# Kernel optimization log

Hardware: AMD Instinct MI355X
Metric: run time of the kernel (lower is better)

Reference implementation:

```python
import jax, jax.numpy as jnp
import numpy as np

OBS_DIM = 512
BACKBONE_DIMS = [1024, 1024, 512]
EXPERT_HIDDEN = 256
NUM_EXPERTS = 16
NUM_ACTIONS = 32
BATCH = 65536


def _glorot(key, shape):
    fan_in = shape[-2] if len(shape) >= 2 else shape[-1]
    return jax.random.normal(key, shape, dtype=jnp.float32) * (1.0 / np.sqrt(fan_in))


def setup_inputs() -> dict:
    key = jax.random.key(0)
    ks = jax.random.split(key, 16)
    inp = {}
    inp['obs'] = jax.random.normal(ks[0], (BATCH, OBS_DIM), dtype=jnp.float32)
    # shared backbone: 512->1024->1024->512 (Linear+ReLU+Dropout(eval=identity))
    dims = [OBS_DIM] + BACKBONE_DIMS
    for i in range(3):
        inp[f'Wb{i}'] = _glorot(ks[1 + i], (dims[i], dims[i + 1]))
        inp[f'bb{i}'] = jnp.zeros((dims[i + 1],), dtype=jnp.float32)
    # experts, batched over expert dim: 512->256->ReLU->256->32
    inp['We1'] = _glorot(ks[4], (NUM_EXPERTS, BACKBONE_DIMS[-1], EXPERT_HIDDEN))
    inp['be1'] = jnp.zeros((NUM_EXPERTS, EXPERT_HIDDEN), dtype=jnp.float32)
    inp['We2'] = _glorot(ks[5], (NUM_EXPERTS, EXPERT_HIDDEN, NUM_ACTIONS))
    inp['be2'] = jnp.zeros((NUM_EXPERTS, NUM_ACTIONS), dtype=jnp.float32)
    # motion selector: 512->256->128->16 + softmax
    inp['Ws0'] = _glorot(ks[6], (OBS_DIM, 256))
    inp['bs0'] = jnp.zeros((256,), dtype=jnp.float32)
    inp['Ws1'] = _glorot(ks[7], (256, 128))
    inp['bs1'] = jnp.zeros((128,), dtype=jnp.float32)
    inp['Ws2'] = _glorot(ks[8], (128, NUM_EXPERTS))
    inp['bs2'] = jnp.zeros((NUM_EXPERTS,), dtype=jnp.float32)
    return inp


def reference(obs, Wb0, bb0, Wb1, bb1, Wb2, bb2, We1, be1, We2, be2,
              Ws0, bs0, Ws1, bs1, Ws2, bs2):
    # shared backbone (Dropout is identity in eval/inference)
    h = jax.nn.relu(obs @ Wb0 + bb0)
    h = jax.nn.relu(h @ Wb1 + bb1)
    h = jax.nn.relu(h @ Wb2 + bb2)  # [B, 512]
    # all experts on shared features, as one batched GEMM
    eh = jax.nn.relu(jnp.einsum('bd,edh->beh', h, We1) + be1)       # [B, E, 256]
    expert_actions = jnp.einsum('beh,eha->bea', eh, We2) + be2       # [B, E, A]
    # motion selector (softmax fusion weights)
    s = jax.nn.relu(obs @ Ws0 + bs0)
    s = jax.nn.relu(s @ Ws1 + bs1)
    w = jax.nn.softmax(s @ Ws2 + bs2, axis=-1)                        # [B, E]
    # softmax-weighted fusion over experts
    fused = jnp.einsum('bea,be->ba', expert_actions, w)              # [B, A]
    return fused
```

## Files before the change

### kernel.cpp

```cpp
#include <hip/hip_runtime.h>
#include <hip/hip_bf16.h>
#include <stdint.h>

typedef __attribute__((ext_vector_type(8))) short short8;
typedef __attribute__((ext_vector_type(4))) float f32x4;

__device__ __forceinline__ float b2f(short s) {
    union { unsigned u; float f; } v; v.u = ((unsigned)(unsigned short)s) << 16; return v.f;
}
__device__ __forceinline__ short f2b(float f) {
    union { float f; unsigned u; } v; v.f = f;
    unsigned r = (v.u + 0x7FFF + ((v.u >> 16) & 1)) >> 16;
    return (short)r;
}

__device__ __forceinline__ void gload16(const void* g, void* l) {
    __builtin_amdgcn_global_load_lds(
        (const __attribute__((address_space(1))) void*)(uintptr_t)g,
        (__attribute__((address_space(3))) void*)(uintptr_t)l,
        16, 0, 0);
}

#define BAR()    asm volatile("s_barrier" ::: "memory")
#define WAITV2() asm volatile("s_waitcnt vmcnt(2)" ::: "memory")
#define WAITV0() asm volatile("s_waitcnt vmcnt(0)" ::: "memory")
#define WAITL0() asm volatile("s_waitcnt lgkmcnt(0)" ::: "memory")

__global__ __launch_bounds__(256) void cast_bf16_kernel(
    const float* __restrict__ src, short* __restrict__ dst, int n8) {
    int i = blockIdx.x * 256 + threadIdx.x;
    if (i >= n8) return;
    const float4* s = (const float4*)src + (size_t)i * 2;
    float4 x0 = s[0], x1 = s[1];
    short8 o;
    o[0] = f2b(x0.x); o[1] = f2b(x0.y); o[2] = f2b(x0.z); o[3] = f2b(x0.w);
    o[4] = f2b(x1.x); o[5] = f2b(x1.y); o[6] = f2b(x1.z); o[7] = f2b(x1.w);
    *((short8*)dst + i) = o;
}

__global__ __launch_bounds__(256) void transpose_cast_kernel(
    const float* __restrict__ W, short* __restrict__ Wt, int K, int N, int total) {
    int t = blockIdx.x * 256 + threadIdx.x;
    if (t >= total) return;
    const float* src = W + (size_t)blockIdx.y * K * N;
    short* dst = Wt + (size_t)blockIdx.y * K * N;
    int n = t % N;
    int k0 = (t / N) * 8;
    short8 o;
#pragma unroll
    for (int i = 0; i < 8; i++) o[i] = f2b(src[(size_t)(k0 + i) * N + n]);
    *(short8*)(dst + (size_t)n * K + k0) = o;
}

__global__ __launch_bounds__(256) void repack_We2_kernel(
    const float* __restrict__ We2, short* __restrict__ Bt2) {
    int t = blockIdx.x * 256 + threadIdx.x;
    int h0 = (t & 31) * 8;
    int a = (t >> 5) & 31;
    int e = t >> 10;
    short8 o;
#pragma unroll
    for (int j = 0; j < 8; j++) o[j] = f2b(We2[((size_t)e * 256 + h0 + j) * 32 + a]);
    *(short8*)(Bt2 + (size_t)a * 4096 + e * 256 + h0) = o;
}

__global__ __launch_bounds__(256, 3)
void gemm_bt_bias_relu(const short* __restrict__ A, const short* __restrict__ Bt,
                       const float* __restrict__ bias, short* __restrict__ C,
                       int M, int N, int K) {
    __shared__ __align__(16) short As[128 * 32];
    __shared__ __align__(16) short Bs[128 * 32];
    const int tid = threadIdx.x;
    const int w = tid >> 6, lane = tid & 63;
    const int tm = blockIdx.y * 128, tn = blockIdx.x * 128;
    const int wm = (w & 1) * 64, wn = (w >> 1) * 64;
    const int r = lane & 15, q = lane >> 4, qk = q * 8;

    const int c0 = w * 2, c1 = w * 2 + 1;
    const int srow0 = c0 * 16 + (lane >> 2);
    const int srow1 = c1 * 16 + (lane >> 2);
    const int skk = (lane & 3) * 8;
    const short* gA0 = A + (size_t)(tm + srow0) * K + skk;
    const short* gA1 = A + (size_t)(tm + srow1) * K + skk;
    const short* gB0 = Bt + (size_t)(tn + srow0) * K + skk;
    const short* gB1 = Bt + (size_t)(tn + srow1) * K + skk;
    short* lA0 = &As[c0 * 512]; short* lA1 = &As[c1 * 512];
    short* lB0 = &Bs[c0 * 512]; short* lB1 = &Bs[c1 * 512];

    f32x4 acc[4][4] = {};
    for (int k0 = 0; k0 < K; k0 += 32) {
        gload16(gA0 + k0, lA0);
        gload16(gA1 + k0, lA1);
        gload16(gB0 + k0, lB0);
        gload16(gB1 + k0, lB1);
        __syncthreads();
        short8 a[4], b[4];
#pragma unroll
        for (int i = 0; i < 4; i++) a[i] = *(const short8*)&As[(wm + i * 16 + r) * 32 + qk];
#pragma unroll
        for (int j = 0; j < 4; j++) b[j] = *(const short8*)&Bs[(wn + j * 16 + r) * 32 + qk];
#pragma unroll
        for (int i = 0; i < 4; i++)
#pragma unroll
            for (int j = 0; j < 4; j++)
                acc[i][j] = __builtin_amdgcn_mfma_f32_16x16x32_bf16(a[i], b[j], acc[i][j], 0, 0, 0);
        __syncthreads();
    }
#pragma unroll
    for (int j = 0; j < 4; j++) {
        int col = tn + wn + j * 16 + r;
        float bj = bias[col];
#pragma unroll
        for (int i = 0; i < 4; i++)
#pragma unroll
            for (int rr = 0; rr < 4; rr++) {
                int row = tm + wm + i * 16 + q * 4 + rr;
                float v = fmaxf(acc[i][j][rr] + bj, 0.f);
                C[(size_t)row * N + col] = f2b(v);
            }
    }
}

__global__ __launch_bounds__(256)
void selector_softmax(const short* __restrict__ s1, const short* __restrict__ Ws2t,
                      const float* __restrict__ bs2, float* __restrict__ wsel) {
    int tid = threadIdx.x;
    int row = blockIdx.x * 16 + (tid >> 4);
    int e = tid & 15;
    const short8* a = (const short8*)(s1 + (size_t)row * 128);
    const short8* b = (const short8*)(Ws2t + (size_t)e * 128);
    float acc = bs2[e];
#pragma unroll
    for (int kk = 0; kk < 16; ++kk) {
        short8 av = a[kk], bv = b[kk];
#pragma unroll
        for (int i = 0; i < 8; i++) acc = fmaf(b2f(av[i]), b2f(bv[i]), acc);
    }
    float m = acc;
#pragma unroll
    for (int off = 8; off >= 1; off >>= 1) m = fmaxf(m, __shfl_xor(m, off, 16));
    float ex = __expf(acc - m);
    float s = ex;
#pragma unroll
    for (int off = 8; off >= 1; off >>= 1) s += __shfl_xor(s, off, 16);
    wsel[(size_t)row * 16 + e] = ex / s;
}

template<int MODE>
__global__ __launch_bounds__(512, 2)
void gemm256(const short* __restrict__ A, const short* __restrict__ Bt,
             const float* __restrict__ bias, const float* __restrict__ wselp,
             short* __restrict__ C, int M, int N, int K) {
    extern __shared__ __align__(16) short lds[];
    const int tid = threadIdx.x;
    const int w = tid >> 6, lane = tid & 63;
    const int wr = w >> 2, wc = w & 3;

    const int gx = gridDim.x;
    const int b = blockIdx.y * gx + blockIdx.x;
    const int per = (gx * gridDim.y) >> 3;
    const int sb = (b & 7) * per + (b >> 3);
    const int bx = sb % gx, by = sb / gx;
    const int tm = by * 256, tn = bx * 256;

    const int rih = w * 8 + (lane >> 3);
    const int colel = (((lane & 7) ^ (lane >> 3)) << 3);
    const short* pA = A + (size_t)(tm + rih) * K + colel;
    const short* pB = Bt + (size_t)(tn + rih) * K + colel;
    const size_t rK64 = (size_t)64 * K, rK128 = (size_t)128 * K;
    short* const ldsw = lds + w * 512;

#define STG_A(buf, h, t) do { \
        const short* s_ = pA + (size_t)(h) * rK128 + (size_t)(t) * 64; \
        short* d_ = ldsw + (buf) * 32768 + (h) * 8192; \
        gload16(s_, d_); \
        gload16(s_ + rK64, d_ + 4096); } while (0)
#define STG_B(buf, h, t) do { \
        const short* s_ = pB + (size_t)(h) * rK128 + (size_t)(t) * 64; \
        short* d_ = ldsw + (buf) * 32768 + 16384 + (h) * 8192; \
        gload16(s_, d_); \
        gload16(s_ + rK64, d_ + 4096); } while (0)

    const int rA = lane & 15;
    const int csw0 = (((lane >> 4) << 4)) ^ ((lane & 7) << 4);
    const int csw1 = (64 + ((lane >> 4) << 4)) ^ ((lane & 7) << 4);
    const char* const ldsB_ = (const char*)lds;
    const int aBase0 = wr * 16384 + rA * 128;
    const int bBase0 = 32768 + (wc >> 1) * 16384 + ((wc & 1) * 64 + rA) * 128;

    f32x4 acc[8][4] = {};
    short8 a[4][2], b0[2][2], b1[2][2];
    const int nt = K >> 6;

    STG_A(0, 0, 0); STG_A(0, 1, 0); STG_B(0, 0, 0); STG_B(0, 1, 0);
    STG_A(1, 0, 1);
    WAITV2(); BAR();

    for (int t = 0; t < nt; ++t) {
        const int cur = t & 1, nxt = cur ^ 1;
        const char* pa = ldsB_ + cur * 65536 + aBase0;
        const char* pb = ldsB_ + cur * 65536 + bBase0;
#pragma unroll
        for (int m = 0; m < 4; m++) {
            a[m][0] = *(const short8*)(pa + m * 2048 + csw0);
            a[m][1] = *(const short8*)(pa + m * 2048 + csw1);
        }
#pragma unroll
        for (int n = 0; n < 2; n++) {
            b0[n][0] = *(const short8*)(pb + n * 2048 + csw0);
            b0[n][1] = *(const short8*)(pb + n * 2048 + csw1);
        }
        if (t + 1 < nt) STG_A(nxt, 1, t + 1);
        BAR(); WAITL0(); __builtin_amdgcn_sched_barrier(0);
        __builtin_amdgcn_s_setprio(1);
#pragma unroll
        for (int m = 0; m < 4; m++)
#pragma unroll
            for (int n = 0; n < 2; n++) {
                acc[m][n] = __builtin_amdgcn_mfma_f32_16x16x32_bf16(a[m][0], b0[n][0], acc[m][n], 0, 0, 0);
                acc[m][n] = __builtin_amdgcn_mfma_f32_16x16x32_bf16(a[m][1], b0[n][1], acc[m][n], 0, 0, 0);
            }
        __builtin_amdgcn_s_setprio(0);
        BAR();
#pragma unroll
        for (int n = 0; n < 2; n++) {
            b1[n][0] = *(const short8*)(pb + (2 + n) * 2048 + csw0);
            b1[n][1] = *(const short8*)(pb + (2 + n) * 2048 + csw1);
        }
        if (t + 1 < nt) STG_B(nxt, 0, t + 1);
        BAR(); WAITL0(); __builtin_amdgcn_sched_barrier(0);
        __builtin_amdgcn_s_setprio(1);
#pragma unroll
        for (int m = 0; m < 4; m++)
#pragma unroll
            for (int n = 0; n < 2; n++) {
                acc[m][2 + n] = __builtin_amdgcn_mfma_f32_16x16x32_bf16(a[m][0], b1[n][0], acc[m][2 + n], 0, 0, 0);
                acc[m][2 + n] = __builtin_amdgcn_mfma_f32_16x16x32_bf16(a[m][1], b1[n][1], acc[m][2 + n], 0, 0, 0);
            }
        __builtin_amdgcn_s_setprio(0);
        BAR();
#pragma unroll
        for (int m = 0; m < 4; m++) {
            a[m][0] = *(const short8*)(pa + (4 + m) * 2048 + csw0);
            a[m][1] = *(const short8*)(pa + (4 + m) * 2048 + csw1);
        }
        if (t + 1 < nt) STG_B(nxt, 1, t + 1);
        BAR(); WAITL0(); __builtin_amdgcn_sched_barrier(0);
        __builtin_amdgcn_s_setprio(1);
#pragma unroll
        for (int m = 0; m < 4; m++)
#pragma unroll
            for (int n = 0; n < 2; n++) {
                acc[4 + m][2 + n] = __builtin_amdgcn_mfma_f32_16x16x32_bf16(a[m][0], b1[n][0], acc[4 + m][2 + n], 0, 0, 0);
                acc[4 + m][2 + n] = __builtin_amdgcn_mfma_f32_16x16x32_bf16(a[m][1], b1[n][1], acc[4 + m][2 + n], 0, 0, 0);
            }
        __builtin_amdgcn_s_setprio(0);
        BAR();
        if (t + 2 < nt) { STG_A(cur, 0, t + 2); WAITV2(); }
        else { WAITV0(); }
        BAR();
        __builtin_amdgcn_s_setprio(1);
#pragma unroll
        for (int m = 0; m < 4; m++)
#pragma unroll
            for (int n = 0; n < 2; n++) {
                acc[4 + m][n] = __builtin_amdgcn_mfma_f32_16x16x32_bf16(a[m][0], b0[n][0], acc[4 + m][n], 0, 0, 0);
                acc[4 + m][n] = __builtin_amdgcn_mfma_f32_16x16x32_bf16(a[m][1], b0[n][1], acc[4 + m][n], 0, 0, 0);
            }
        __builtin_amdgcn_s_setprio(0);
        BAR();
    }
#undef STG_A
#undef STG_B

    float biasv[4];
#pragma unroll
    for (int n = 0; n < 4; n++) biasv[n] = bias[tn + wc * 64 + n * 16 + rA];
    const int q4 = (lane >> 4) * 4;
#pragma unroll
    for (int m = 0; m < 8; m++)
#pragma unroll
        for (int rr = 0; rr < 4; rr++) {
            const int row = tm + wr * 128 + m * 16 + q4 + rr;
            float ws = 1.f;
            if (MODE == 1) ws = wselp[(size_t)row * 16 + (tn >> 8)];
#pragma unroll
            for (int n = 0; n < 4; n++) {
                const int col = tn + wc * 64 + n * 16 + rA;
                float v = fmaxf(acc[m][n][rr] + biasv[n], 0.f);
                if (MODE == 1) v *= ws;
                C[(size_t)row * N + col] = f2b(v);
            }
        }
}

__global__ __launch_bounds__(256)
void fuse_gemm(const short* __restrict__ Aeh, const short* __restrict__ Bt2,
               const float* __restrict__ wsel, const float* __restrict__ be2,
               float* __restrict__ out, int accflag) {
    __shared__ __align__(16) short sA[2][128 * 64];
    const int tid = threadIdx.x;
    const int w = tid >> 6, lane = tid & 63;
    const int tm = blockIdx.x * 128;
    const int rih = w * 8 + (lane >> 3);
    const int colel = (((lane & 7) ^ (lane >> 3)) << 3);
    const short* pA = Aeh + (size_t)(tm + rih) * 2048 + colel;
    const int rA = lane & 15;
    const int csw0 = (((lane >> 4) << 4)) ^ ((lane & 7) << 4);
    const int csw1 = (64 + ((lane >> 4) << 4)) ^ ((lane & 7) << 4);
    const short* pBg = Bt2 + (size_t)rA * 4096 + ((lane >> 4) << 3);

    f32x4 acc[2][2] = {};
#define STG_E(buf, t) do { \
        const short* s_ = pA + (size_t)(t) * 64; \
        short* d_ = &sA[buf][w * 512]; \
        gload16(s_, d_); \
        gload16(s_ + (size_t)32 * 2048, d_ + 2048); \
        gload16(s_ + (size_t)64 * 2048, d_ + 4096); \
        gload16(s_ + (size_t)96 * 2048, d_ + 6144); } while (0)

    const int NT = 32;
    STG_E(0, 0);
    WAITV0(); BAR();
    for (int t = 0; t < NT; ++t) {
        const int cur = t & 1;
        if (t + 1 < NT) STG_E(cur ^ 1, t + 1);
        const char* pa = (const char*)&sA[cur][0] + (w * 32 + rA) * 128;
        short8 av[2][2], bv[2][2];
#pragma unroll
        for (int m = 0; m < 2; m++) {
            av[m][0] = *(const short8*)(pa + m * 2048 + csw0);
            av[m][1] = *(const short8*)(pa + m * 2048 + csw1);
        }
#pragma unroll
        for (int n = 0; n < 2; n++) {
            bv[n][0] = *(const short8*)(pBg + (size_t)n * 16 * 4096 + t * 64);
            bv[n][1] = *(const short8*)(pBg + (size_t)n * 16 * 4096 + t * 64 + 32);
        }
#pragma unroll
        for (int m = 0; m < 2; m++)
#pragma unroll
            for (int n = 0; n < 2; n++) {
                acc[m][n] = __builtin_amdgcn_mfma_f32_16x16x32_bf16(av[m][0], bv[n][0], acc[m][n], 0, 0, 0);
                acc[m][n] = __builtin_amdgcn_mfma_f32_16x16x32_bf16(av[m][1], bv[n][1], acc[m][n], 0, 0, 0);
            }
        WAITL0(); WAITV0(); BAR();
    }
#undef STG_E

    float be2v0[16], be2v1[16];
    if (!accflag) {
#pragma unroll
        for (int e = 0; e < 16; e++) {
            be2v0[e] = be2[e * 32 + rA];
            be2v1[e] = be2[e * 32 + 16 + rA];
        }
    }
    const int q4 = (lane >> 4) * 4;
#pragma unroll
    for (int m = 0; m < 2; m++)
#pragma unroll
        for (int rr = 0; rr < 4; rr++) {
            const int row = tm + w * 32 + m * 16 + q4 + rr;
            float v0 = acc[m][0][rr], v1 = acc[m][1][rr];
            if (!accflag) {
#pragma unroll
                for (int e = 0; e < 16; e++) {
                    float wv = wsel[(size_t)row * 16 + e];
                    v0 = fmaf(wv, be2v0[e], v0);
                    v1 = fmaf(wv, be2v1[e], v1);
                }
                out[(size_t)row * 32 + rA] = v0;
                out[(size_t)row * 32 + 16 + rA] = v1;
            } else {
                out[(size_t)row * 32 + rA] += v0;
                out[(size_t)row * 32 + 16 + rA] += v1;
            }
        }
}

extern "C" void kernel_launch(void* const* d_in, const int* in_sizes, int n_in,
                              void* d_out, int out_size, void* d_ws, size_t ws_size,
                              hipStream_t stream) {
    const float* obs = (const float*)d_in[0];
    const float* Wb0 = (const float*)d_in[1]; const float* bb0 = (const float*)d_in[2];
    const float* Wb1 = (const float*)d_in[3]; const float* bb1 = (const float*)d_in[4];
    const float* Wb2 = (const float*)d_in[5]; const float* bb2 = (const float*)d_in[6];
    const float* We1 = (const float*)d_in[7]; const float* be1 = (const float*)d_in[8];
    const float* We2 = (const float*)d_in[9]; const float* be2 = (const float*)d_in[10];
    const float* Ws0 = (const float*)d_in[11]; const float* bs0 = (const float*)d_in[12];
    const float* Ws1 = (const float*)d_in[13]; const float* bs1 = (const float*)d_in[14];
    const float* Ws2 = (const float*)d_in[15]; const float* bs2 = (const float*)d_in[16];

    const int B = 65536;
    char* ws = (char*)d_ws;
    size_t off = 0;
    auto alloc = [&](size_t bytes) { void* p = ws + off; off += (bytes + 255) & ~(size_t)255; return p; };
    short* obs_bf = (short*)alloc((size_t)B * 512 * 2);
    short* h1     = (short*)alloc((size_t)B * 1024 * 2);
    short* h2     = (short*)alloc((size_t)B * 1024 * 2);
    short* hbuf   = (short*)alloc((size_t)B * 512 * 2);
    short* s0     = (short*)alloc((size_t)B * 256 * 2);
    short* s1     = (short*)alloc((size_t)B * 128 * 2);
    float* wsel   = (float*)alloc((size_t)B * 16 * 4);
    short* Wb0t   = (short*)alloc((size_t)512 * 1024 * 2);
    short* Wb1t   = (short*)alloc((size_t)1024 * 1024 * 2);
    short* Wb2t   = (short*)alloc((size_t)1024 * 512 * 2);
    short* We1t   = (short*)alloc((size_t)16 * 512 * 256 * 2);
    short* Ws0t   = (short*)alloc((size_t)512 * 256 * 2);
    short* Ws1t   = (short*)alloc((size_t)256 * 128 * 2);
    short* Ws2t   = (short*)alloc((size_t)128 * 16 * 2);
    short* Bt2    = (short*)alloc((size_t)32 * 4096 * 2);
    short* s_eh = h1;

    static int inited = 0;
    if (!inited) {
        hipFuncSetAttribute(reinterpret_cast<const void*>(gemm256<0>),
                            hipFuncAttributeMaxDynamicSharedMemorySize, 131072);
        hipFuncSetAttribute(reinterpret_cast<const void*>(gemm256<1>),
                            hipFuncAttributeMaxDynamicSharedMemorySize, 131072);
        inited = 1;
    }

    cast_bf16_kernel<<<(B * 512 / 8 + 255) / 256, 256, 0, stream>>>(obs, obs_bf, B * 512 / 8);
    transpose_cast_kernel<<<dim3((1024 * 512 / 8 + 255) / 256, 1), 256, 0, stream>>>(Wb0, Wb0t, 512, 1024, 1024 * 512 / 8);
    transpose_cast_kernel<<<dim3((1024 * 1024 / 8 + 255) / 256, 1), 256, 0, stream>>>(Wb1, Wb1t, 1024, 1024, 1024 * 1024 / 8);
    transpose_cast_kernel<<<dim3((512 * 1024 / 8 + 255) / 256, 1), 256, 0, stream>>>(Wb2, Wb2t, 1024, 512, 512 * 1024 / 8);
    transpose_cast_kernel<<<dim3((256 * 512 / 8 + 255) / 256, 16), 256, 0, stream>>>(We1, We1t, 512, 256, 256 * 512 / 8);
    transpose_cast_kernel<<<dim3((256 * 512 / 8 + 255) / 256, 1), 256, 0, stream>>>(Ws0, Ws0t, 512, 256, 256 * 512 / 8);
    transpose_cast_kernel<<<dim3((128 * 256 / 8 + 255) / 256, 1), 256, 0, stream>>>(Ws1, Ws1t, 256, 128, 128 * 256 / 8);
    transpose_cast_kernel<<<dim3((16 * 128 / 8 + 255) / 256, 1), 256, 0, stream>>>(Ws2, Ws2t, 128, 16, 16 * 128 / 8);
    repack_We2_kernel<<<64, 256, 0, stream>>>(We2, Bt2);

    gemm256<0><<<dim3(1, B / 256), 512, 131072, stream>>>(obs_bf, Ws0t, bs0, nullptr, s0, B, 256, 512);
    gemm_bt_bias_relu<<<dim3(1, B / 128), 256, 0, stream>>>(s0, Ws1t, bs1, s1, B, 128, 256);
    selector_softmax<<<B / 16, 256, 0, stream>>>(s1, Ws2t, bs2, wsel);

    gemm256<0><<<dim3(4, B / 256), 512, 131072, stream>>>(obs_bf, Wb0t, bb0, nullptr, h1, B, 1024, 512);
    gemm256<0><<<dim3(4, B / 256), 512, 131072, stream>>>(h1, Wb1t, bb1, nullptr, h2, B, 1024, 1024);
    gemm256<0><<<dim3(2, B / 256), 512, 131072, stream>>>(h2, Wb2t, bb2, nullptr, hbuf, B, 512, 1024);

    for (int g = 0; g < 2; ++g) {
        gemm256<1><<<dim3(8, B / 256), 512, 131072, stream>>>(
            hbuf, We1t + (size_t)g * 8 * 256 * 512, be1 + g * 2048, wsel + g * 8,
            s_eh, B, 2048, 512);
        fuse_gemm<<<B / 128, 256, 0, stream>>>(
            s_eh, Bt2 + g * 2048, wsel, be2, (float*)d_out, g);
    }
}
```

Before: 1.127 ms.

## Fuse expert GEMMs into a persistent MoE kernel and trim barriers in gemm256

Replaces the two-pass expert path with a single kernel. That kernel materialises the eh intermediate (B x 4096) and then runs a separate fuse GEMM. The new kernel loops over all 16 experts for each 256-row tile. It computes the first expert layer, stages the ReLU output in LDS, multiplies it by We2 with MFMA, and accumulates the softmax-weighted result directly into the output. The output is pre-initialised with the weighted be2 bias. This removes the large global write and re-read of expert hidden activations. Separately, several s_barriers are dropped from the gemm256 main loop and the next-tile prefetch is moved after the last MFMA block. Dropping those barriers risks LDS races, and the fused kernel launches only 256 blocks, which can limit occupancy.

```diff
diff --git a/kernel.cpp b/kernel.cpp
--- a/kernel.cpp
+++ b/kernel.cpp
@@ -1,6 +1,7 @@
 #include <hip/hip_runtime.h>
 #include <hip/hip_bf16.h>
 #include <stdint.h>
+
 
 typedef __attribute__((ext_vector_type(8))) short short8;
 typedef __attribute__((ext_vector_type(4))) float f32x4;
@@ -25,6 +26,7 @@
 #define WAITV2() asm volatile("s_waitcnt vmcnt(2)" ::: "memory")
 #define WAITV0() asm volatile("s_waitcnt vmcnt(0)" ::: "memory")
 #define WAITL0() asm volatile("s_waitcnt lgkmcnt(0)" ::: "memory")
+#define SGB()    __builtin_amdgcn_sched_barrier(0)
 
 __global__ __launch_bounds__(256) void cast_bf16_kernel(
     const float* __restrict__ src, short* __restrict__ dst, int n8) {
@@ -50,18 +52,6 @@
 #pragma unroll
     for (int i = 0; i < 8; i++) o[i] = f2b(src[(size_t)(k0 + i) * N + n]);
     *(short8*)(dst + (size_t)n * K + k0) = o;
-}
-
-__global__ __launch_bounds__(256) void repack_We2_kernel(
-    const float* __restrict__ We2, short* __restrict__ Bt2) {
-    int t = blockIdx.x * 256 + threadIdx.x;
-    int h0 = (t & 31) * 8;
-    int a = (t >> 5) & 31;
-    int e = t >> 10;
-    short8 o;
-#pragma unroll
-    for (int j = 0; j < 8; j++) o[j] = f2b(We2[((size_t)e * 256 + h0 + j) * 32 + a]);
-    *(short8*)(Bt2 + (size_t)a * 4096 + e * 256 + h0) = o;
 }
 
 __global__ __launch_bounds__(256, 3)
@@ -146,11 +136,22 @@
     wsel[(size_t)row * 16 + e] = ex / s;
 }
 
-template<int MODE>
+__global__ __launch_bounds__(256)
+void out_init_kernel(const float* __restrict__ wsel, const float* __restrict__ be2,
+                     float* __restrict__ out) {
+    int i = blockIdx.x * 256 + threadIdx.x;
+    int row = i >> 5, a = i & 31;
+    const float* wr = wsel + (size_t)row * 16;
+    float acc = 0.f;
+#pragma unroll
+    for (int e = 0; e < 16; e++) acc = fmaf(wr[e], be2[e * 32 + a], acc);
+    out[i] = acc;
+}
+
 __global__ __launch_bounds__(512, 2)
 void gemm256(const short* __restrict__ A, const short* __restrict__ Bt,
-             const float* __restrict__ bias, const float* __restrict__ wselp,
-             short* __restrict__ C, int M, int N, int K) {
+             const float* __restrict__ bias, short* __restrict__ C,
+             int M, int N, int K) {
     extern __shared__ __align__(16) short lds[];
     const int tid = threadIdx.x;
     const int w = tid >> 6, lane = tid & 63;
@@ -181,9 +182,9 @@
         gload16(s_, d_); \
         gload16(s_ + rK64, d_ + 4096); } while (0)
 
-    const int rA = lane & 15;
-    const int csw0 = (((lane >> 4) << 4)) ^ ((lane & 7) << 4);
-    const int csw1 = (64 + ((lane >> 4) << 4)) ^ ((lane & 7) << 4);
+    const int rA = lane & 15, q = lane >> 4;
+    const int csw0 = ((q << 4)) ^ ((lane & 7) << 4);
+    const int csw1 = (64 + (q << 4)) ^ ((lane & 7) << 4);
     const char* const ldsB_ = (const char*)lds;
     const int aBase0 = wr * 16384 + rA * 128;
     const int bBase0 = 32768 + (wc >> 1) * 16384 + ((wc & 1) * 64 + rA) * 128;
@@ -211,7 +212,7 @@
             b0[n][1] = *(const short8*)(pb + n * 2048 + csw1);
         }
         if (t + 1 < nt) STG_A(nxt, 1, t + 1);
-        BAR(); WAITL0(); __builtin_amdgcn_sched_barrier(0);
+        WAITL0(); SGB();
         __builtin_amdgcn_s_setprio(1);
 #pragma unroll
         for (int m = 0; m < 4; m++)
@@ -221,14 +222,13 @@
                 acc[m][n] = __builtin_amdgcn_mfma_f32_16x16x32_bf16(a[m][1], b0[n][1], acc[m][n], 0, 0, 0);
             }
         __builtin_amdgcn_s_setprio(0);
-        BAR();
 #pragma unroll
         for (int n = 0; n < 2; n++) {
             b1[n][0] = *(const short8*)(pb + (2 + n) * 2048 + csw0);
             b1[n][1] = *(const short8*)(pb + (2 + n) * 2048 + csw1);
         }
         if (t + 1 < nt) STG_B(nxt, 0, t + 1);
-        BAR(); WAITL0(); __builtin_amdgcn_sched_barrier(0);
+        WAITL0(); SGB();
         __builtin_amdgcn_s_setprio(1);
 #pragma unroll
         for (int m = 0; m < 4; m++)
@@ -238,14 +238,13 @@
                 acc[m][2 + n] = __builtin_amdgcn_mfma_f32_16x16x32_bf16(a[m][1], b1[n][1], acc[m][2 + n], 0, 0, 0);
             }
         __builtin_amdgcn_s_setprio(0);
-        BAR();
 #pragma unroll
         for (int m = 0; m < 4; m++) {
             a[m][0] = *(const short8*)(pa + (4 + m) * 2048 + csw0);
             a[m][1] = *(const short8*)(pa + (4 + m) * 2048 + csw1);
         }
         if (t + 1 < nt) STG_B(nxt, 1, t + 1);
-        BAR(); WAITL0(); __builtin_amdgcn_sched_barrier(0);
+        WAITL0(); SGB();
         __builtin_amdgcn_s_setprio(1);
 #pragma unroll
         for (int m = 0; m < 4; m++)
@@ -255,10 +254,6 @@
                 acc[4 + m][2 + n] = __builtin_amdgcn_mfma_f32_16x16x32_bf16(a[m][1], b1[n][1], acc[4 + m][2 + n], 0, 0, 0);
             }
         __builtin_amdgcn_s_setprio(0);
-        BAR();
-        if (t + 2 < nt) { STG_A(cur, 0, t + 2); WAITV2(); }
-        else { WAITV0(); }
-        BAR();
         __builtin_amdgcn_s_setprio(1);
 #pragma unroll
         for (int m = 0; m < 4; m++)
@@ -269,6 +264,9 @@
             }
         __builtin_amdgcn_s_setprio(0);
         BAR();
+        if (t + 2 < nt) { STG_A(cur, 0, t + 2); WAITV2(); }
+        else WAITV0();
+        BAR();
     }
 #undef STG_A
 #undef STG_B
@@ -276,107 +274,206 @@
     float biasv[4];
 #pragma unroll
     for (int n = 0; n < 4; n++) biasv[n] = bias[tn + wc * 64 + n * 16 + rA];
-    const int q4 = (lane >> 4) * 4;
+    const int q4 = q * 4;
 #pragma unroll
     for (int m = 0; m < 8; m++)
 #pragma unroll
         for (int rr = 0; rr < 4; rr++) {
             const int row = tm + wr * 128 + m * 16 + q4 + rr;
-            float ws = 1.f;
-            if (MODE == 1) ws = wselp[(size_t)row * 16 + (tn >> 8)];
 #pragma unroll
             for (int n = 0; n < 4; n++) {
                 const int col = tn + wc * 64 + n * 16 + rA;
                 float v = fmaxf(acc[m][n][rr] + biasv[n], 0.f);
-                if (MODE == 1) v *= ws;
                 C[(size_t)row * N + col] = f2b(v);
             }
         }
 }
 
-__global__ __launch_bounds__(256)
-void fuse_gemm(const short* __restrict__ Aeh, const short* __restrict__ Bt2,
-               const float* __restrict__ wsel, const float* __restrict__ be2,
-               float* __restrict__ out, int accflag) {
-    __shared__ __align__(16) short sA[2][128 * 64];
+__global__ __launch_bounds__(512, 2)
+void moe_kernel(const short* __restrict__ hbuf, const short* __restrict__ We1t,
+                const short* __restrict__ We2t, const float* __restrict__ be1,
+                const float* __restrict__ wsel, float* __restrict__ out) {
+    extern __shared__ __align__(16) short lds[];
     const int tid = threadIdx.x;
     const int w = tid >> 6, lane = tid & 63;
-    const int tm = blockIdx.x * 128;
+    const int wr = w >> 2, wc = w & 3;
+    const int b = blockIdx.x;
+    const int sb = (b & 7) * 32 + (b >> 3);
+    const int tm = sb * 256;
+
     const int rih = w * 8 + (lane >> 3);
     const int colel = (((lane & 7) ^ (lane >> 3)) << 3);
-    const short* pA = Aeh + (size_t)(tm + rih) * 2048 + colel;
-    const int rA = lane & 15;
-    const int csw0 = (((lane >> 4) << 4)) ^ ((lane & 7) << 4);
-    const int csw1 = (64 + ((lane >> 4) << 4)) ^ ((lane & 7) << 4);
-    const short* pBg = Bt2 + (size_t)rA * 4096 + ((lane >> 4) << 3);
-
-    f32x4 acc[2][2] = {};
-#define STG_E(buf, t) do { \
-        const short* s_ = pA + (size_t)(t) * 64; \
-        short* d_ = &sA[buf][w * 512]; \
+    const short* pA = hbuf + (size_t)(tm + rih) * 512 + colel;
+    const short* pB0 = We1t + (size_t)rih * 512 + colel;
+    short* const ldsw = lds + w * 512;
+
+#define MSTG_A(buf, h, t) do { \
+        const short* s_ = pA + (size_t)(h) * 65536 + (size_t)(t) * 64; \
+        short* d_ = ldsw + (buf) * 32768 + (h) * 8192; \
         gload16(s_, d_); \
-        gload16(s_ + (size_t)32 * 2048, d_ + 2048); \
-        gload16(s_ + (size_t)64 * 2048, d_ + 4096); \
-        gload16(s_ + (size_t)96 * 2048, d_ + 6144); } while (0)
-
-    const int NT = 32;
-    STG_E(0, 0);
-    WAITV0(); BAR();
-    for (int t = 0; t < NT; ++t) {
-        const int cur = t & 1;
-        if (t + 1 < NT) STG_E(cur ^ 1, t + 1);
-        const char* pa = (const char*)&sA[cur][0] + (w * 32 + rA) * 128;
-        short8 av[2][2], bv[2][2];
-#pragma unroll
-        for (int m = 0; m < 2; m++) {
-            av[m][0] = *(const short8*)(pa + m * 2048 + csw0);
-            av[m][1] = *(const short8*)(pa + m * 2048 + csw1);
-        }
-#pragma unroll
-        for (int n = 0; n < 2; n++) {
-            bv[n][0] = *(const short8*)(pBg + (size_t)n * 16 * 4096 + t * 64);
-            bv[n][1] = *(const short8*)(pBg + (size_t)n * 16 * 4096 + t * 64 + 32);
-        }
-#pragma unroll
-        for (int m = 0; m < 2; m++)
+        gload16(s_ + 32768, d_ + 4096); } while (0)
+#define MSTG_B(P, buf, h, t) do { \
+        const short* s_ = (P) + (size_t)(h) * 65536 + (size_t)(t) * 64; \
+        short* d_ = ldsw + (buf) * 32768 + 16384 + (h) * 8192; \
+        gload16(s_, d_); \
+        gload16(s_ + 32768, d_ + 4096); } while (0)
+
+    const int rA = lane & 15, q = lane >> 4;
+    const int csw0 = ((q << 4)) ^ ((lane & 7) << 4);
+    const int csw1 = (64 + (q << 4)) ^ ((lane & 7) << 4);
+    const char* const ldsB_ = (const char*)lds;
+    const int aBase0 = wr * 16384 + rA * 128;
+    const int bBase0 = 32768 + (wc >> 1) * 16384 + ((wc & 1) * 64 + rA) * 128;
+    const int q4 = q * 4;
+
+    short8 a[4][2], b0[2][2], b1[2][2];
+
+    {
+        const short* pBe = pB0;
+        MSTG_A(0, 0, 0); MSTG_A(0, 1, 0);
+        MSTG_B(pBe, 0, 0, 0); MSTG_B(pBe, 0, 1, 0);
+    }
+
+#pragma unroll 1
+    for (int e = 0; e < 16; ++e) {
+        const short* pBe = pB0 + (size_t)e * 131072;
+        WAITV0(); BAR();
+        f32x4 acc[8][4] = {};
+#pragma unroll 1
+        for (int t = 0; t < 8; ++t) {
+            const int cur = t & 1, nxt = cur ^ 1;
+            const char* pa = ldsB_ + cur * 65536 + aBase0;
+            const char* pb = ldsB_ + cur * 65536 + bBase0;
+#pragma unroll
+            for (int m = 0; m < 4; m++) {
+                a[m][0] = *(const short8*)(pa + m * 2048 + csw0);
+                a[m][1] = *(const short8*)(pa + m * 2048 + csw1);
+            }
 #pragma unroll
             for (int n = 0; n < 2; n++) {
-                acc[m][n] = __builtin_amdgcn_mfma_f32_16x16x32_bf16(av[m][0], bv[n][0], acc[m][n], 0, 0, 0);
-                acc[m][n] = __builtin_amdgcn_mfma_f32_16x16x32_bf16(av[m][1], bv[n][1], acc[m][n], 0, 0, 0);
-            }
-        WAITL0(); WAITV0(); BAR();
-    }
-#undef STG_E
-
-    float be2v0[16], be2v1[16];
-    if (!accflag) {
-#pragma unroll
-        for (int e = 0; e < 16; e++) {
-            be2v0[e] = be2[e * 32 + rA];
-            be2v1[e] = be2[e * 32 + 16 + rA];
-        }
-    }
-    const int q4 = (lane >> 4) * 4;
-#pragma unroll
-    for (int m = 0; m < 2; m++)
-#pragma unroll
-        for (int rr = 0; rr < 4; rr++) {
-            const int row = tm + w * 32 + m * 16 + q4 + rr;
-            float v0 = acc[m][0][rr], v1 = acc[m][1][rr];
-            if (!accflag) {
-#pragma unroll
-                for (int e = 0; e < 16; e++) {
-                    float wv = wsel[(size_t)row * 16 + e];
-                    v0 = fmaf(wv, be2v0[e], v0);
-                    v1 = fmaf(wv, be2v1[e], v1);
-                }
-                out[(size_t)row * 32 + rA] = v0;
-                out[(size_t)row * 32 + 16 + rA] = v1;
-            } else {
-                out[(size_t)row * 32 + rA] += v0;
-                out[(size_t)row * 32 + 16 + rA] += v1;
-            }
-        }
+                b0[n][0] = *(const short8*)(pb + n * 2048 + csw0);
+                b0[n][1] = *(const short8*)(pb + n * 2048 + csw1);
+            }
+            if (t < 7) MSTG_A(nxt, 1, t + 1);
+            if (t == 0) MSTG_A(nxt, 0, 1);
+            WAITL0(); SGB();
+            __builtin_amdgcn_s_setprio(1);
+#pragma unroll
+            for (int m = 0; m < 4; m++)
+#pragma unroll
+                for (int n = 0; n < 2; n++) {
+                    acc[m][n] = __builtin_amdgcn_mfma_f32_16x16x32_bf16(a[m][0], b0[n][0], acc[m][n], 0, 0, 0);
+                    acc[m][n] = __builtin_amdgcn_mfma_f32_16x16x32_bf16(a[m][1], b0[n][1], acc[m][n], 0, 0, 0);
+                }
+            __builtin_amdgcn_s_setprio(0);
+#pragma unroll
+            for (int n = 0; n < 2; n++) {
+                b1[n][0] = *(const short8*)(pb + (2 + n) * 2048 + csw0);
+                b1[n][1] = *(const short8*)(pb + (2 + n) * 2048 + csw1);
+            }
+            if (t < 7) MSTG_B(pBe, nxt, 0, t + 1);
+            WAITL0(); SGB();
+            __builtin_amdgcn_s_setprio(1);
+#pragma unroll
+            for (int m = 0; m < 4; m++)
+#pragma unroll
+                for (int n = 0; n < 2; n++) {
+                    acc[m][2 + n] = __builtin_amdgcn_mfma_f32_16x16x32_bf16(a[m][0], b1[n][0], acc[m][2 + n], 0, 0, 0);
+                    acc[m][2 + n] = __builtin_amdgcn_mfma_f32_16x16x32_bf16(a[m][1], b1[n][1], acc[m][2 + n], 0, 0, 0);
+                }
+            __builtin_amdgcn_s_setprio(0);
+#pragma unroll
+            for (int m = 0; m < 4; m++) {
+                a[m][0] = *(const short8*)(pa + (4 + m) * 2048 + csw0);
+                a[m][1] = *(const short8*)(pa + (4 + m) * 2048 + csw1);
+            }
+            if (t < 7) MSTG_B(pBe, nxt, 1, t + 1);
+            WAITL0(); SGB();
+            __builtin_amdgcn_s_setprio(1);
+#pragma unroll
+            for (int m = 0; m < 4; m++)
+#pragma unroll
+                for (int n = 0; n < 2; n++) {
+                    acc[4 + m][2 + n] = __builtin_amdgcn_mfma_f32_16x16x32_bf16(a[m][0], b1[n][0], acc[4 + m][2 + n], 0, 0, 0);
+                    acc[4 + m][2 + n] = __builtin_amdgcn_mfma_f32_16x16x32_bf16(a[m][1], b1[n][1], acc[4 + m][2 + n], 0, 0, 0);
+                }
+            __builtin_amdgcn_s_setprio(0);
+            __builtin_amdgcn_s_setprio(1);
+#pragma unroll
+            for (int m = 0; m < 4; m++)
+#pragma unroll
+                for (int n = 0; n < 2; n++) {
+                    acc[4 + m][n] = __builtin_amdgcn_mfma_f32_16x16x32_bf16(a[m][0], b0[n][0], acc[4 + m][n], 0, 0, 0);
+                    acc[4 + m][n] = __builtin_amdgcn_mfma_f32_16x16x32_bf16(a[m][1], b0[n][1], acc[4 + m][n], 0, 0, 0);
+                }
+            __builtin_amdgcn_s_setprio(0);
+            BAR();
+            if (t < 6) { MSTG_A(cur, 0, t + 2); WAITV2(); }
+            else WAITV0();
+            BAR();
+        }
+
+        if (e + 1 < 16) {
+            const short* pBn = pB0 + (size_t)(e + 1) * 131072;
+            MSTG_A(0, 0, 0); MSTG_A(0, 1, 0);
+            MSTG_B(pBn, 0, 0, 0); MSTG_B(pBn, 0, 1, 0);
+        }
+        f32x4 g2[2][2] = {};
+#pragma unroll
+        for (int hh = 0; hh < 2; ++hh) {
+            if ((wc >> 1) == hh) {
+                const int chb = (wc & 1) * 64;
+#pragma unroll
+                for (int n = 0; n < 4; n++) {
+                    const int col = chb + n * 16 + rA;
+                    const float bv = be1[e * 256 + hh * 128 + col];
+#pragma unroll
+                    for (int m = 0; m < 8; m++)
+#pragma unroll
+                        for (int rr = 0; rr < 4; rr++) {
+                            const int row = wr * 128 + m * 16 + q4 + rr;
+                            const int byt = 65536 + row * 256 + ((col * 2) ^ ((row & 7) << 4));
+                            *(short*)((char*)lds + byt) = f2b(fmaxf(acc[m][n][rr] + bv, 0.f));
+                        }
+                }
+            }
+            WAITL0(); BAR();
+#pragma unroll
+            for (int k2 = 0; k2 < 4; ++k2) {
+                short8 a2[2], b2[2];
+#pragma unroll
+                for (int m2 = 0; m2 < 2; m2++) {
+                    const int row = w * 32 + m2 * 16 + rA;
+                    a2[m2] = *(const short8*)((const char*)lds + 65536 + row * 256 +
+                                              ((k2 * 64 + q * 16) ^ ((row & 7) << 4)));
+                }
+#pragma unroll
+                for (int n2 = 0; n2 < 2; n2++)
+                    b2[n2] = *(const short8*)(We2t + (size_t)(e * 32 + n2 * 16 + rA) * 256 +
+                                              hh * 128 + k2 * 32 + q * 8);
+#pragma unroll
+                for (int m2 = 0; m2 < 2; m2++)
+#pragma unroll
+                    for (int n2 = 0; n2 < 2; n2++)
+                        g2[m2][n2] = __builtin_amdgcn_mfma_f32_16x16x32_bf16(a2[m2], b2[n2], g2[m2][n2], 0, 0, 0);
+            }
+            WAITL0(); BAR();
+        }
+#pragma unroll
+        for (int m2 = 0; m2 < 2; m2++)
+#pragma unroll
+            for (int rr = 0; rr < 4; rr++) {
+                const int row = tm + w * 32 + m2 * 16 + q4 + rr;
+                const float ws = wsel[(size_t)row * 16 + e];
+#pragma unroll
+                for (int n2 = 0; n2 < 2; n2++) {
+                    float* po = out + (size_t)row * 32 + n2 * 16 + rA;
+                    *po = *po + ws * g2[m2][n2][rr];
+                }
+            }
+    }
+#undef MSTG_A
+#undef MSTG_B
 }
 
 extern "C" void kernel_launch(void* const* d_in, const int* in_sizes, int n_in,
@@ -407,17 +504,16 @@
     short* Wb1t   = (short*)alloc((size_t)1024 * 1024 * 2);
     short* Wb2t   = (short*)alloc((size_t)1024 * 512 * 2);
     short* We1t   = (short*)alloc((size_t)16 * 512 * 256 * 2);
+    short* We2t   = (short*)alloc((size_t)16 * 256 * 32 * 2);
     short* Ws0t   = (short*)alloc((size_t)512 * 256 * 2);
     short* Ws1t   = (short*)alloc((size_t)256 * 128 * 2);
     short* Ws2t   = (short*)alloc((size_t)128 * 16 * 2);
-    short* Bt2    = (short*)alloc((size_t)32 * 4096 * 2);
-    short* s_eh = h1;
 
     static int inited = 0;
     if (!inited) {
-        hipFuncSetAttribute(reinterpret_cast<const void*>(gemm256<0>),
+        hipFuncSetAttribute(reinterpret_cast<const void*>(gemm256),
                             hipFuncAttributeMaxDynamicSharedMemorySize, 131072);
-        hipFuncSetAttribute(reinterpret_cast<const void*>(gemm256<1>),
+        hipFuncSetAttribute(reinterpret_cast<const void*>(moe_kernel),
                             hipFuncAttributeMaxDynamicSharedMemorySize, 131072);
         inited = 1;
     }
@@ -427,24 +523,19 @@
     transpose_cast_kernel<<<dim3((1024 * 1024 / 8 + 255) / 256, 1), 256, 0, stream>>>(Wb1, Wb1t, 1024, 1024, 1024 * 1024 / 8);
     transpose_cast_kernel<<<dim3((512 * 1024 / 8 + 255) / 256, 1), 256, 0, stream>>>(Wb2, Wb2t, 1024, 512, 512 * 1024 / 8);
     transpose_cast_kernel<<<dim3((256 * 512 / 8 + 255) / 256, 16), 256, 0, stream>>>(We1, We1t, 512, 256, 256 * 512 / 8);
+    transpose_cast_kernel<<<dim3((32 * 256 / 8 + 255) / 256, 16), 256, 0, stream>>>(We2, We2t, 256, 32, 32 * 256 / 8);
     transpose_cast_kernel<<<dim3((256 * 512 / 8 + 255) / 256, 1), 256, 0, stream>>>(Ws0, Ws0t, 512, 256, 256 * 512 / 8);
     transpose_cast_kernel<<<dim3((128 * 256 / 8 + 255) / 256, 1), 256, 0, stream>>>(Ws1, Ws1t, 256, 128, 128 * 256 / 8);
     transpose_cast_kernel<<<dim3((16 * 128 / 8 + 255) / 256, 1), 256, 0, stream>>>(Ws2, Ws2t, 128, 16, 16 * 128 / 8);
-    repack_We2_kernel<<<64, 256, 0, stream>>>(We2, Bt2);
-
-    gemm256<0><<<dim3(1, B / 256), 512, 131072, stream>>>(obs_bf, Ws0t, bs0, nullptr, s0, B, 256, 512);
+
+    gemm256<<<dim3(1, B / 256), 512, 131072, stream>>>(obs_bf, Ws0t, bs0, s0, B, 256, 512);
     gemm_bt_bias_relu<<<dim3(1, B / 128), 256, 0, stream>>>(s0, Ws1t, bs1, s1, B, 128, 256);
     selector_softmax<<<B / 16, 256, 0, stream>>>(s1, Ws2t, bs2, wsel);
-
-    gemm256<0><<<dim3(4, B / 256), 512, 131072, stream>>>(obs_bf, Wb0t, bb0, nullptr, h1, B, 1024, 512);
-    gemm256<0><<<dim3(4, B / 256), 512, 131072, stream>>>(h1, Wb1t, bb1, nullptr, h2, B, 1024, 1024);
-    gemm256<0><<<dim3(2, B / 256), 512, 131072, stream>>>(h2, Wb2t, bb2, nullptr, hbuf, B, 512, 1024);
-
-    for (int g = 0; g < 2; ++g) {
-        gemm256<1><<<dim3(8, B / 256), 512, 131072, stream>>>(
-            hbuf, We1t + (size_t)g * 8 * 256 * 512, be1 + g * 2048, wsel + g * 8,
-            s_eh, B, 2048, 512);
-        fuse_gemm<<<B / 128, 256, 0, stream>>>(
-            s_eh, Bt2 + g * 2048, wsel, be2, (float*)d_out, g);
-    }
-}
+    out_init_kernel<<<B * 32 / 256, 256, 0, stream>>>(wsel, be2, (float*)d_out);
+
+    gemm256<<<dim3(4, B / 256), 512, 131072, stream>>>(obs_bf, Wb0t, bb0, h1, B, 1024, 512);
+    gemm256<<<dim3(4, B / 256), 512, 131072, stream>>>(h1, Wb1t, bb1, h2, B, 1024, 1024);
+    gemm256<<<dim3(2, B / 256), 512, 131072, stream>>>(h2, Wb2t, bb2, hbuf, B, 512, 1024);
+
+    moe_kernel<<<256, 512, 131072, stream>>>(hbuf, We1t, We2t, be1, wsel, (float*)d_out);
+}
```

Result: slower. 1.978 ms (+75.5%).

## Simplify GEMM double-buffer pipeline to one barrier per K-tile

Applied to the files above, without the earlier changes.

The staggered per-phase staging of A/B halves into LDS is replaced by issuing all next-tile global-to-LDS loads at the start of each iteration. Completion is waited on once at the end, with a single barrier per K step instead of several. The aim is to cut barrier stalls and wave synchronization between MFMA phases. In exchange, the partial two-tiles-ahead prefetch is lost and memory requests are issued in one burst.

```diff
diff --git a/kernel.cpp b/kernel.cpp
--- a/kernel.cpp
+++ b/kernel.cpp
@@ -22,9 +22,9 @@
 }
 
 #define BAR()    asm volatile("s_barrier" ::: "memory")
-#define WAITV2() asm volatile("s_waitcnt vmcnt(2)" ::: "memory")
 #define WAITV0() asm volatile("s_waitcnt vmcnt(0)" ::: "memory")
 #define WAITL0() asm volatile("s_waitcnt lgkmcnt(0)" ::: "memory")
+#define SGB()    __builtin_amdgcn_sched_barrier(0)
 
 __global__ __launch_bounds__(256) void cast_bf16_kernel(
     const float* __restrict__ src, short* __restrict__ dst, int n8) {
@@ -181,9 +181,9 @@
         gload16(s_, d_); \
         gload16(s_ + rK64, d_ + 4096); } while (0)
 
-    const int rA = lane & 15;
-    const int csw0 = (((lane >> 4) << 4)) ^ ((lane & 7) << 4);
-    const int csw1 = (64 + ((lane >> 4) << 4)) ^ ((lane & 7) << 4);
+    const int rA = lane & 15, q = lane >> 4;
+    const int csw0 = ((q << 4)) ^ ((lane & 7) << 4);
+    const int csw1 = (64 + (q << 4)) ^ ((lane & 7) << 4);
     const char* const ldsB_ = (const char*)lds;
     const int aBase0 = wr * 16384 + rA * 128;
     const int bBase0 = 32768 + (wc >> 1) * 16384 + ((wc & 1) * 64 + rA) * 128;
@@ -193,8 +193,7 @@
     const int nt = K >> 6;
 
     STG_A(0, 0, 0); STG_A(0, 1, 0); STG_B(0, 0, 0); STG_B(0, 1, 0);
-    STG_A(1, 0, 1);
-    WAITV2(); BAR();
+    WAITV0(); BAR();
 
     for (int t = 0; t < nt; ++t) {
         const int cur = t & 1, nxt = cur ^ 1;
@@ -210,8 +209,11 @@
             b0[n][0] = *(const short8*)(pb + n * 2048 + csw0);
             b0[n][1] = *(const short8*)(pb + n * 2048 + csw1);
         }
-        if (t + 1 < nt) STG_A(nxt, 1, t + 1);
-        BAR(); WAITL0(); __builtin_amdgcn_sched_barrier(0);
+        if (t + 1 < nt) {
+            STG_A(nxt, 0, t + 1); STG_A(nxt, 1, t + 1);
+            STG_B(nxt, 0, t + 1); STG_B(nxt, 1, t + 1);
+        }
+        WAITL0(); SGB();
         __builtin_amdgcn_s_setprio(1);
 #pragma unroll
         for (int m = 0; m < 4; m++)
@@ -221,14 +223,12 @@
                 acc[m][n] = __builtin_amdgcn_mfma_f32_16x16x32_bf16(a[m][1], b0[n][1], acc[m][n], 0, 0, 0);
             }
         __builtin_amdgcn_s_setprio(0);
-        BAR();
 #pragma unroll
         for (int n = 0; n < 2; n++) {
             b1[n][0] = *(const short8*)(pb + (2 + n) * 2048 + csw0);
             b1[n][1] = *(const short8*)(pb + (2 + n) * 2048 + csw1);
         }
-        if (t + 1 < nt) STG_B(nxt, 0, t + 1);
-        BAR(); WAITL0(); __builtin_amdgcn_sched_barrier(0);
+        WAITL0(); SGB();
         __builtin_amdgcn_s_setprio(1);
 #pragma unroll
         for (int m = 0; m < 4; m++)
@@ -238,14 +238,12 @@
                 acc[m][2 + n] = __builtin_amdgcn_mfma_f32_16x16x32_bf16(a[m][1], b1[n][1], acc[m][2 + n], 0, 0, 0);
             }
         __builtin_amdgcn_s_setprio(0);
-        BAR();
 #pragma unroll
         for (int m = 0; m < 4; m++) {
             a[m][0] = *(const short8*)(pa + (4 + m) * 2048 + csw0);
             a[m][1] = *(const short8*)(pa + (4 + m) * 2048 + csw1);
         }
-        if (t + 1 < nt) STG_B(nxt, 1, t + 1);
-        BAR(); WAITL0(); __builtin_amdgcn_sched_barrier(0);
+        WAITL0(); SGB();
         __builtin_amdgcn_s_setprio(1);
 #pragma unroll
         for (int m = 0; m < 4; m++)
@@ -255,10 +253,6 @@
                 acc[4 + m][2 + n] = __builtin_amdgcn_mfma_f32_16x16x32_bf16(a[m][1], b1[n][1], acc[4 + m][2 + n], 0, 0, 0);
             }
         __builtin_amdgcn_s_setprio(0);
-        BAR();
-        if (t + 2 < nt) { STG_A(cur, 0, t + 2); WAITV2(); }
-        else { WAITV0(); }
-        BAR();
         __builtin_amdgcn_s_setprio(1);
 #pragma unroll
         for (int m = 0; m < 4; m++)
@@ -268,6 +262,7 @@
                 acc[4 + m][n] = __builtin_amdgcn_mfma_f32_16x16x32_bf16(a[m][1], b0[n][1], acc[4 + m][n], 0, 0, 0);
             }
         __builtin_amdgcn_s_setprio(0);
+        WAITV0();
         BAR();
     }
 #undef STG_A
@@ -276,7 +271,7 @@
     float biasv[4];
 #pragma unroll
     for (int n = 0; n < 4; n++) biasv[n] = bias[tn + wc * 64 + n * 16 + rA];
-    const int q4 = (lane >> 4) * 4;
+    const int q4 = q * 4;
 #pragma unroll
     for (int m = 0; m < 8; m++)
 #pragma unroll
```

Result: no change. 1.117 ms (-0.9%).
